# Kernel optimization log

Measured on AMD Instinct MI355X. Metric: run time of the kernel, lower is better.

Reference implementation:

```python
import jax, jax.numpy as jnp
import numpy as np

L, B, T, D, H, DH, DFF, S = 4, 64, 511, 1024, 16, 64, 4096, 256
SCALE = 1.0 / np.sqrt(DH)
EPS = 1e-5


def _ln(x, g, b):
    m = x.mean(-1, keepdims=True)
    v = ((x - m) ** 2).mean(-1, keepdims=True)
    return (x - m) * jax.lax.rsqrt(v + EPS) * g + b


def setup_inputs() -> dict:
    key = jax.random.key(0)
    ks = jax.random.split(key, 24)
    wp = 0.02  # weight init scale to keep activations sane
    r = lambda k, shp, s: jax.random.normal(k, shp, jnp.float32) * s
    return {
        'tgt_last': r(ks[0], (1, B, D), 1.0),
        'cache': r(ks[1], (L, T, B, D), 1.0),
        'K0': r(ks[2], (B, H, T, DH), 1.0),
        'V0': r(ks[3], (B, H, T, DH), 1.0),
        'K_mem': r(ks[4], (L, B, H, S, DH), 1.0),
        'V_mem': r(ks[5], (L, B, H, S, DH), 1.0),
        'sa_W': r(ks[6], (L, 3 * D, D), wp), 'sa_b': r(ks[7], (L, 3 * D), wp),
        'sa_oW': r(ks[8], (L, D, D), wp), 'sa_ob': r(ks[9], (L, D), wp),
        'ca_qW': r(ks[10], (L, D, D), wp), 'ca_qb': r(ks[11], (L, D), wp),
        'ca_oW': r(ks[12], (L, D, D), wp), 'ca_ob': r(ks[13], (L, D), wp),
        'W1': r(ks[14], (L, DFF, D), wp), 'b1': r(ks[15], (L, DFF), wp),
        'W2': r(ks[16], (L, D, DFF), wp), 'b2': r(ks[17], (L, D), wp),
        'ln1_g': jnp.ones((L, D), jnp.float32), 'ln1_b': jnp.zeros((L, D), jnp.float32),
        'ln2_g': jnp.ones((L, D), jnp.float32), 'ln2_b': jnp.zeros((L, D), jnp.float32),
        'ln3_g': jnp.ones((L, D), jnp.float32), 'ln3_b': jnp.zeros((L, D), jnp.float32),
    }


def reference(tgt_last, cache, K0, V0, K_mem, V_mem, sa_W, sa_b, sa_oW, sa_ob,
              ca_qW, ca_qb, ca_oW, ca_ob, W1, b1, W2, b2,
              ln1_g, ln1_b, ln2_g, ln2_b, ln3_g, ln3_b):
    # One incremental decode step through L decoder layers (eval mode, dropout=0).
    x = tgt_last  # [1,B,D]
    for i in range(L):
        last = x
        Wq, Wk, Wv = sa_W[i, :D], sa_W[i, D:2 * D], sa_W[i, 2 * D:]
        bq, bk, bv = sa_b[i, :D], sa_b[i, D:2 * D], sa_b[i, 2 * D:]
        q = (last[0] @ Wq.T + bq).reshape(B, H, DH)  # [B,H,Dh]
        if i == 0:
            # _sa_kv_step: project only the new token, append to cached K/V
            k = (last[0] @ Wk.T + bk).reshape(B, H, 1, DH)
            v = (last[0] @ Wv.T + bv).reshape(B, H, 1, DH)
            K = jnp.concatenate([K0, k], axis=2)  # [B,H,T+1,Dh]
            V = jnp.concatenate([V0, v], axis=2)
        else:
            # standard self-attn: K/V from full prefix concat(cache[i], x)
            tgt_i = jnp.concatenate([cache[i], x], axis=0)  # [T+1,B,D]
            K = (tgt_i @ Wk.T + bk).reshape(T + 1, B, H, DH).transpose(1, 2, 0, 3)
            V = (tgt_i @ Wv.T + bv).reshape(T + 1, B, H, DH).transpose(1, 2, 0, 3)
        s = jnp.einsum('bhd,bhtd->bht', q, K) * SCALE
        a = jax.nn.softmax(s, axis=-1)
        ctx = jnp.einsum('bht,bhtd->bhd', a, V).reshape(B, D)[None]  # [1,B,D]
        sa = ctx @ sa_oW[i].T + sa_ob[i]
        x = _ln(last + sa, ln1_g[i], ln1_b[i])
        # cross-attention against precomputed memory K/V
        qc = (x[0] @ ca_qW[i].T + ca_qb[i]).reshape(B, H, DH)
        sc = jnp.einsum('bhd,bhsd->bhs', qc, K_mem[i]) * SCALE
        ac = jax.nn.softmax(sc, axis=-1)
        cc = jnp.einsum('bhs,bhsd->bhd', ac, V_mem[i]).reshape(B, D)[None]
        cc = cc @ ca_oW[i].T + ca_ob[i]
        x = _ln(x + cc, ln2_g[i], ln2_b[i])
        # FFN (relu, the nn.TransformerDecoderLayer default)
        ff = jax.nn.relu(x @ W1[i].T + b1[i]) @ W2[i].T + b2[i]
        x = _ln(x + ff, ln3_g[i], ln3_b[i])
    return x  # [1,B,D] embedding of the newly decoded token
```

## Files before the change

kernel.cpp:

```cpp
#include <hip/hip_runtime.h>
#include <math.h>

#define B 64
#define D 1024
#define H 16
#define DH 64
#define T 511
#define TT 512
#define SMEM 256
#define DFF 4096
#define NLAYER 4
#define SCALE 0.125f
#define EPS 1e-5f

__device__ __forceinline__ float dot4(const float4 a, const float4 b) {
    return a.x * b.x + a.y * b.y + a.z * b.z + a.w * b.w;
}
__device__ __forceinline__ float4 f4add(float4 a, float4 b) {
    return make_float4(a.x + b.x, a.y + b.y, a.z + b.z, a.w + b.w);
}

template <int K, int KS>
__global__ __launch_bounds__(256) void gemm_proj(
    const float* __restrict__ A,
    const float* __restrict__ W,
    float* __restrict__ P)
{
    constexpr int KSUB = K / KS;
    const int O = gridDim.x * 128;
    const int obase = blockIdx.x * 128;
    const int kb = blockIdx.y * KSUB;
    const int tid = threadIdx.x;

    __shared__ float As[32][68];
    __shared__ float Ws[32][132];

    const int b0 = (tid >> 4) * 4;
    const int o0 = (tid & 15) * 8;

    float acc[4][8];
#pragma unroll
    for (int i = 0; i < 4; ++i)
#pragma unroll
        for (int j = 0; j < 8; ++j) acc[i][j] = 0.f;

    for (int kc = 0; kc < KSUB; kc += 32) {
#pragma unroll
        for (int j = 0; j < 2; ++j) {
            const int f = tid + 256 * j;
            const int bb = f >> 3, k4 = f & 7;
            const float4 v = *reinterpret_cast<const float4*>(
                A + (size_t)bb * K + kb + kc + 4 * k4);
            As[4 * k4 + 0][bb] = v.x; As[4 * k4 + 1][bb] = v.y;
            As[4 * k4 + 2][bb] = v.z; As[4 * k4 + 3][bb] = v.w;
        }
#pragma unroll
        for (int j = 0; j < 4; ++j) {
            const int f = tid + 256 * j;
            const int oo = f >> 3, k4 = f & 7;
            const float4 v = *reinterpret_cast<const float4*>(
                W + (size_t)(obase + oo) * K + kb + kc + 4 * k4);
            Ws[4 * k4 + 0][oo] = v.x; Ws[4 * k4 + 1][oo] = v.y;
            Ws[4 * k4 + 2][oo] = v.z; Ws[4 * k4 + 3][oo] = v.w;
        }
        __syncthreads();
#pragma unroll 8
        for (int k = 0; k < 32; ++k) {
            const float4 av = *reinterpret_cast<const float4*>(&As[k][b0]);
            const float4 w0 = *reinterpret_cast<const float4*>(&Ws[k][o0]);
            const float4 w1 = *reinterpret_cast<const float4*>(&Ws[k][o0 + 4]);
            const float a[4] = {av.x, av.y, av.z, av.w};
            const float w[8] = {w0.x, w0.y, w0.z, w0.w, w1.x, w1.y, w1.z, w1.w};
#pragma unroll
            for (int i = 0; i < 4; ++i)
#pragma unroll
                for (int j = 0; j < 8; ++j)
                    acc[i][j] = fmaf(a[i], w[j], acc[i][j]);
        }
        __syncthreads();
    }

    float* Pb = P + (size_t)blockIdx.y * 64 * O;
#pragma unroll
    for (int i = 0; i < 4; ++i) {
        const float4 v0 = make_float4(acc[i][0], acc[i][1], acc[i][2], acc[i][3]);
        const float4 v1 = make_float4(acc[i][4], acc[i][5], acc[i][6], acc[i][7]);
        *reinterpret_cast<float4*>(Pb + (size_t)(b0 + i) * O + obase + o0) = v0;
        *reinterpret_cast<float4*>(Pb + (size_t)(b0 + i) * O + obase + o0 + 4) = v1;
    }
}

template <int K, int KS, int NPART, bool RELU_A>
__global__ __launch_bounds__(256) void gemm_psum(
    const float* __restrict__ Pa,
    const float* __restrict__ abias,
    const float* __restrict__ W,
    float* __restrict__ P)
{
    constexpr int KSUB = K / KS;
    const int O = gridDim.x * 128;
    const int obase = blockIdx.x * 128;
    const int kb = blockIdx.y * KSUB;
    const int tid = threadIdx.x;

    __shared__ float As[32][68];
    __shared__ float Ws[32][132];

    const int b0 = (tid >> 4) * 4;
    const int o0 = (tid & 15) * 8;

    float acc[4][8];
#pragma unroll
    for (int i = 0; i < 4; ++i)
#pragma unroll
        for (int j = 0; j < 8; ++j) acc[i][j] = 0.f;

    for (int kc = 0; kc < KSUB; kc += 32) {
#pragma unroll
        for (int j = 0; j < 2; ++j) {
            const int f = tid + 256 * j;
            const int bb = f >> 3, k4 = f & 7;
            const int kg = kb + kc + 4 * k4;
            float4 v = *reinterpret_cast<const float4*>(abias + kg);
#pragma unroll
            for (int s = 0; s < NPART; ++s)
                v = f4add(v, *reinterpret_cast<const float4*>(
                    Pa + (size_t)(s * 64 + bb) * K + kg));
            if (RELU_A) {
                v.x = fmaxf(v.x, 0.f); v.y = fmaxf(v.y, 0.f);
                v.z = fmaxf(v.z, 0.f); v.w = fmaxf(v.w, 0.f);
            }
            As[4 * k4 + 0][bb] = v.x; As[4 * k4 + 1][bb] = v.y;
            As[4 * k4 + 2][bb] = v.z; As[4 * k4 + 3][bb] = v.w;
        }
#pragma unroll
        for (int j = 0; j < 4; ++j) {
            const int f = tid + 256 * j;
            const int oo = f >> 3, k4 = f & 7;
            const float4 v = *reinterpret_cast<const float4*>(
                W + (size_t)(obase + oo) * K + kb + kc + 4 * k4);
            Ws[4 * k4 + 0][oo] = v.x; Ws[4 * k4 + 1][oo] = v.y;
            Ws[4 * k4 + 2][oo] = v.z; Ws[4 * k4 + 3][oo] = v.w;
        }
        __syncthreads();
#pragma unroll 8
        for (int k = 0; k < 32; ++k) {
            const float4 av = *reinterpret_cast<const float4*>(&As[k][b0]);
            const float4 w0 = *reinterpret_cast<const float4*>(&Ws[k][o0]);
            const float4 w1 = *reinterpret_cast<const float4*>(&Ws[k][o0 + 4]);
            const float a[4] = {av.x, av.y, av.z, av.w};
            const float w[8] = {w0.x, w0.y, w0.z, w0.w, w1.x, w1.y, w1.z, w1.w};
#pragma unroll
            for (int i = 0; i < 4; ++i)
#pragma unroll
                for (int j = 0; j < 8; ++j)
                    acc[i][j] = fmaf(a[i], w[j], acc[i][j]);
        }
        __syncthreads();
    }

    float* Pb = P + (size_t)blockIdx.y * 64 * O;
#pragma unroll
    for (int i = 0; i < 4; ++i) {
        const float4 v0 = make_float4(acc[i][0], acc[i][1], acc[i][2], acc[i][3]);
        const float4 v1 = make_float4(acc[i][4], acc[i][5], acc[i][6], acc[i][7]);
        *reinterpret_cast<float4*>(Pb + (size_t)(b0 + i) * O + obase + o0) = v0;
        *reinterpret_cast<float4*>(Pb + (size_t)(b0 + i) * O + obase + o0 + 4) = v1;
    }
}

__global__ __launch_bounds__(256) void gemm_u(
    const float* __restrict__ Pq,
    const float* __restrict__ bq,
    const float* __restrict__ Wk,
    float* __restrict__ u)
{
    const int h = blockIdx.x;
    const int dbase = blockIdx.y * 128;
    const int tid = threadIdx.x;

    __shared__ float As[32][68];
    __shared__ float Ws[32][132];

    const int b0 = (tid >> 4) * 4;
    const int o0 = (tid & 15) * 8;

    float acc[4][8];
#pragma unroll
    for (int i = 0; i < 4; ++i)
#pragma unroll
        for (int j = 0; j < 8; ++j) acc[i][j] = 0.f;

    for (int kc = 0; kc < DH; kc += 32) {
#pragma unroll
        for (int j = 0; j < 2; ++j) {
            const int f = tid + 256 * j;
            const int bb = f >> 3, k4 = f & 7;
            const int kg = h * DH + kc + 4 * k4;
            float4 v = *reinterpret_cast<const float4*>(bq + kg);
#pragma unroll
            for (int s = 0; s < 16; ++s)
                v = f4add(v, *reinterpret_cast<const float4*>(
                    Pq + (size_t)(s * 64 + bb) * D + kg));
            As[4 * k4 + 0][bb] = v.x; As[4 * k4 + 1][bb] = v.y;
            As[4 * k4 + 2][bb] = v.z; As[4 * k4 + 3][bb] = v.w;
        }
#pragma unroll
        for (int j = 0; j < 4; ++j) {
            const int f = tid + 256 * j;
            const int k = f >> 5, d4 = f & 31;
            const float4 v = *reinterpret_cast<const float4*>(
                Wk + (size_t)(h * DH + kc + k) * D + dbase + 4 * d4);
            *reinterpret_cast<float4*>(&Ws[k][4 * d4]) = v;
        }
        __syncthreads();
#pragma unroll 8
        for (int k = 0; k < 32; ++k) {
            const float4 av = *reinterpret_cast<const float4*>(&As[k][b0]);
            const float4 w0 = *reinterpret_cast<const float4*>(&Ws[k][o0]);
            const float4 w1 = *reinterpret_cast<const float4*>(&Ws[k][o0 + 4]);
            const float a[4] = {av.x, av.y, av.z, av.w};
            const float w[8] = {w0.x, w0.y, w0.z, w0.w, w1.x, w1.y, w1.z, w1.w};
#pragma unroll
            for (int i = 0; i < 4; ++i)
#pragma unroll
                for (int j = 0; j < 8; ++j)
                    acc[i][j] = fmaf(a[i], w[j], acc[i][j]);
        }
        __syncthreads();
    }
#pragma unroll
    for (int i = 0; i < 4; ++i) {
        const float4 v0 = make_float4(acc[i][0], acc[i][1], acc[i][2], acc[i][3]);
        const float4 v1 = make_float4(acc[i][4], acc[i][5], acc[i][6], acc[i][7]);
        float* ur = u + ((size_t)(b0 + i) * H + h) * D + dbase + o0;
        *reinterpret_cast<float4*>(ur) = v0;
        *reinterpret_cast<float4*>(ur + 4) = v1;
    }
}

__global__ __launch_bounds__(512) void sattn_kernel(
    const float* __restrict__ cache_i, const float* __restrict__ x,
    const float* __restrict__ u, float* __restrict__ wpart4,
    float* __restrict__ sums)
{
    const int b = blockIdx.x, th = blockIdx.y;
    const int tid = threadIdx.x;
    const int h = tid >> 5, seg = tid & 31;

    float4 ur[8];
    const float* ub = u + ((size_t)(b * H + h)) * D;
#pragma unroll
    for (int c = 0; c < 8; ++c) {
        const float4 v = *reinterpret_cast<const float4*>(ub + c * 128 + seg * 4);
        ur[c] = make_float4(v.x * SCALE, v.y * SCALE, v.z * SCALE, v.w * SCALE);
    }
    float4 ar[8];
#pragma unroll
    for (int c = 0; c < 8; ++c) ar[c] = make_float4(0.f, 0.f, 0.f, 0.f);
    float sumE = 0.f;

    __shared__ float rowb[2][2][1024];

    const int tg0 = th * 128;
    const int lr = tid >> 8;
    const int lc = (tid & 255) * 4;

    auto rowptr = [&](int t) -> const float* {
        return (t < T) ? cache_i + ((size_t)t * B + b) * D : x + (size_t)b * D;
    };
    float4 pre = *reinterpret_cast<const float4*>(rowptr(tg0 + lr) + lc);

    for (int st = 0; st < 64; ++st) {
        const int p = st & 1;
        *reinterpret_cast<float4*>(&rowb[p][lr][lc]) = pre;
        __syncthreads();
        if (st + 1 < 64)
            pre = *reinterpret_cast<const float4*>(
                rowptr(tg0 + 2 * (st + 1) + lr) + lc);
#pragma unroll
        for (int r = 0; r < 2; ++r) {
            float4 rv[8];
            float dot = 0.f;
#pragma unroll
            for (int c = 0; c < 8; ++c) {
                rv[c] = *reinterpret_cast<const float4*>(
                    &rowb[p][r][c * 128 + seg * 4]);
                dot += dot4(ur[c], rv[c]);
            }
#pragma unroll
            for (int m = 16; m >= 1; m >>= 1) dot += __shfl_xor(dot, m, 64);
            const float e = __expf(dot);
            sumE += e;
#pragma unroll
            for (int c = 0; c < 8; ++c) {
                ar[c].x = fmaf(e, rv[c].x, ar[c].x);
                ar[c].y = fmaf(e, rv[c].y, ar[c].y);
                ar[c].z = fmaf(e, rv[c].z, ar[c].z);
                ar[c].w = fmaf(e, rv[c].w, ar[c].w);
            }
        }
    }

    float* wp = wpart4 + (((size_t)(b * 4 + th)) * H + h) * D;
#pragma unroll
    for (int c = 0; c < 8; ++c)
        *reinterpret_cast<float4*>(wp + c * 128 + seg * 4) = ar[c];
    if (seg == 0) sums[(b * 4 + th) * H + h] = sumE;
}

__global__ __launch_bounds__(256) void gemm_ctx8(
    const float* __restrict__ wpart4, const float* __restrict__ sums,
    const float* __restrict__ Wv, float* __restrict__ P)
{
    constexpr int KSUB = D / 8;
    const int h = blockIdx.x;
    const int kb = blockIdx.y * KSUB;
    const int tid = threadIdx.x;

    __shared__ float As[32][68];
    __shared__ float Ws[32][68];
    __shared__ float sinv[64];

    if (tid < 64) {
        float s = 0.f;
#pragma unroll
        for (int t = 0; t < 4; ++t) s += sums[(tid * 4 + t) * H + h];
        sinv[tid] = 1.f / s;
    }
    __syncthreads();

    const int b0 = (tid >> 4) * 4;
    const int o0 = (tid & 15) * 4;

    float acc[4][4];
#pragma unroll
    for (int i = 0; i < 4; ++i)
#pragma unroll
        for (int j = 0; j < 4; ++j) acc[i][j] = 0.f;

    for (int kc = 0; kc < KSUB; kc += 32) {
#pragma unroll
        for (int j = 0; j < 2; ++j) {
            const int f = tid + 256 * j;
            const int bb = f >> 3, k4 = f & 7;
            const int kg = kb + kc + 4 * k4;
            float4 v = make_float4(0.f, 0.f, 0.f, 0.f);
#pragma unroll
            for (int t = 0; t < 4; ++t)
                v = f4add(v, *reinterpret_cast<const float4*>(
                    wpart4 + (((size_t)(bb * 4 + t)) * H + h) * D + kg));
            const float iv = sinv[bb];
            As[4 * k4 + 0][bb] = v.x * iv; As[4 * k4 + 1][bb] = v.y * iv;
            As[4 * k4 + 2][bb] = v.z * iv; As[4 * k4 + 3][bb] = v.w * iv;
        }
#pragma unroll
        for (int j = 0; j < 2; ++j) {
            const int f = tid + 256 * j;
            const int oo = f >> 3, k4 = f & 7;
            const float4 v = *reinterpret_cast<const float4*>(
                Wv + (size_t)(h * DH + oo) * D + kb + kc + 4 * k4);
            Ws[4 * k4 + 0][oo] = v.x; Ws[4 * k4 + 1][oo] = v.y;
            Ws[4 * k4 + 2][oo] = v.z; Ws[4 * k4 + 3][oo] = v.w;
        }
        __syncthreads();
#pragma unroll 8
        for (int k = 0; k < 32; ++k) {
            const float4 av = *reinterpret_cast<const float4*>(&As[k][b0]);
            const float4 wv = *reinterpret_cast<const float4*>(&Ws[k][o0]);
            const float a[4] = {av.x, av.y, av.z, av.w};
            const float w[4] = {wv.x, wv.y, wv.z, wv.w};
#pragma unroll
            for (int i = 0; i < 4; ++i)
#pragma unroll
                for (int j = 0; j < 4; ++j)
                    acc[i][j] = fmaf(a[i], w[j], acc[i][j]);
        }
        __syncthreads();
    }
    float* Pb = P + (size_t)blockIdx.y * 64 * D;
#pragma unroll
    for (int i = 0; i < 4; ++i) {
        const float4 v = make_float4(acc[i][0], acc[i][1], acc[i][2], acc[i][3]);
        *reinterpret_cast<float4*>(Pb + (size_t)(b0 + i) * D + h * DH + o0) = v;
    }
}

template <int KS>
__global__ __launch_bounds__(256) void finish_ln(
    const float* __restrict__ P, const float* __restrict__ bias,
    const float* __restrict__ resid, const float* __restrict__ g,
    const float* __restrict__ bb, float* __restrict__ out)
{
    const int b = blockIdx.x, tid = threadIdx.x;
    const float4* P4 = reinterpret_cast<const float4*>(P);
    float4 v = reinterpret_cast<const float4*>(bias)[tid];
    v = f4add(v, reinterpret_cast<const float4*>(resid + (size_t)b * D)[tid]);
#pragma unroll
    for (int s = 0; s < KS; ++s)
        v = f4add(v, P4[(size_t)(s * 64 + b) * 256 + tid]);

    float ssum = v.x + v.y + v.z + v.w;
#pragma unroll
    for (int m = 32; m >= 1; m >>= 1) ssum += __shfl_xor(ssum, m, 64);
    __shared__ float red[4];
    if ((tid & 63) == 0) red[tid >> 6] = ssum;
    __syncthreads();
    const float mean = (red[0] + red[1] + red[2] + red[3]) * (1.f / D);
    const float dx = v.x - mean, dy = v.y - mean, dz = v.z - mean, dw = v.w - mean;
    float q = dx * dx + dy * dy + dz * dz + dw * dw;
#pragma unroll
    for (int m = 32; m >= 1; m >>= 1) q += __shfl_xor(q, m, 64);
    __shared__ float red2[4];
    if ((tid & 63) == 0) red2[tid >> 6] = q;
    __syncthreads();
    const float var = (red2[0] + red2[1] + red2[2] + red2[3]) * (1.f / D);
    const float rs = rsqrtf(var + EPS);
    const float4 gv = reinterpret_cast<const float4*>(g)[tid];
    const float4 bv = reinterpret_cast<const float4*>(bb)[tid];
    float4 o;
    o.x = dx * rs * gv.x + bv.x;
    o.y = dy * rs * gv.y + bv.y;
    o.z = dz * rs * gv.z + bv.z;
    o.w = dw * rs * gv.w + bv.w;
    reinterpret_cast<float4*>(out + (size_t)b * D)[tid] = o;
}

template <int NS, bool HASX>
__global__ __launch_bounds__(256) void attn_kernel(
    const float* __restrict__ qP, const float* __restrict__ qbias,
    int qnp, int qpitch,
    const float* __restrict__ Kb, const float* __restrict__ Vb,
    float* __restrict__ ctx, int nk)
{
    const int b = blockIdx.x, h = blockIdx.y, tid = threadIdx.x;
    __shared__ float qs[DH];
    __shared__ float kx[DH];
    __shared__ float vx[DH];
    __shared__ float sa[NS];
    if (tid < DH) {
        const int col = h * DH + tid;
        float v = qbias[col];
        for (int s = 0; s < qnp; ++s)
            v += qP[(size_t)(s * 64 + b) * qpitch + col];
        qs[tid] = v;
        if (HASX) {
            float kk = qbias[D + col];
            float vv = qbias[2 * D + col];
            for (int s = 0; s < qnp; ++s) {
                const float* base = qP + (size_t)(s * 64 + b) * qpitch + col;
                kk += base[D];
                vv += base[2 * D];
            }
            kx[tid] = kk; vx[tid] = vv;
        }
    }
    __syncthreads();

    const int ss = tid >> 2, p = tid & 3;
    const float* Kbh = Kb + ((size_t)(b * H + h)) * nk * DH;
#pragma unroll 2
    for (int pass = 0; pass < NS / 64; ++pass) {
        const int s = pass * 64 + ss;
        const float* row = (!HASX || s < nk) ? (Kbh + (size_t)s * DH)
                                             : (const float*)kx;
        const float4* rp = reinterpret_cast<const float4*>(row);
        const float4* qp = reinterpret_cast<const float4*>(qs) + p * 4;
        float acc = 0.f;
#pragma unroll
        for (int c = 0; c < 4; ++c) acc += dot4(rp[p * 4 + c], qp[c]);
        acc += __shfl_xor(acc, 1, 64);
        acc += __shfl_xor(acc, 2, 64);
        if (p == 0) sa[s] = acc * SCALE;
    }
    __syncthreads();

    float m = -1e30f;
    for (int k = tid; k < NS; k += 256) m = fmaxf(m, sa[k]);
#pragma unroll
    for (int mm = 32; mm >= 1; mm >>= 1) m = fmaxf(m, __shfl_xor(m, mm, 64));
    __shared__ float r1[4];
    if ((tid & 63) == 0) r1[tid >> 6] = m;
    __syncthreads();
    m = fmaxf(fmaxf(r1[0], r1[1]), fmaxf(r1[2], r1[3]));
    float sum = 0.f;
    for (int k = tid; k < NS; k += 256) {
        const float e = __expf(sa[k] - m);
        sa[k] = e;
        sum += e;
    }
#pragma unroll
    for (int mm = 32; mm >= 1; mm >>= 1) sum += __shfl_xor(sum, mm, 64);
    __shared__ float r2[4];
    if ((tid & 63) == 0) r2[tid >> 6] = sum;
    __syncthreads();
    const float inv = 1.f / (r2[0] + r2[1] + r2[2] + r2[3]);

    const int dh4 = tid & 15, sq = tid >> 4;
    const float* Vbh = Vb + ((size_t)(b * H + h)) * nk * DH;
    float4 acc = make_float4(0.f, 0.f, 0.f, 0.f);
#pragma unroll 2
    for (int s = sq; s < NS; s += 16) {
        const float* row = (!HASX || s < nk) ? (Vbh + (size_t)s * DH)
                                             : (const float*)vx;
        const float4 vv = *reinterpret_cast<const float4*>(row + dh4 * 4);
        const float av = sa[s];
        acc.x += av * vv.x; acc.y += av * vv.y;
        acc.z += av * vv.z; acc.w += av * vv.w;
    }
    __shared__ float red[16 * 68];
    *reinterpret_cast<float4*>(&red[sq * 68 + dh4 * 4]) = acc;
    __syncthreads();
    if (tid < 64) {
        float t = 0.f;
#pragma unroll
        for (int k = 0; k < 16; ++k) t += red[k * 68 + tid];
        ctx[(size_t)b * D + h * DH + tid] = t * inv;
    }
}

extern "C" void kernel_launch(void* const* d_in, const int* in_sizes, int n_in,
                              void* d_out, int out_size, void* d_ws, size_t ws_size,
                              hipStream_t stream)
{
    const float* tgt_last = (const float*)d_in[0];
    const float* cache    = (const float*)d_in[1];
    const float* K0       = (const float*)d_in[2];
    const float* V0       = (const float*)d_in[3];
    const float* K_mem    = (const float*)d_in[4];
    const float* V_mem    = (const float*)d_in[5];
    const float* sa_W     = (const float*)d_in[6];
    const float* sa_b     = (const float*)d_in[7];
    const float* sa_oW    = (const float*)d_in[8];
    const float* sa_ob    = (const float*)d_in[9];
    const float* ca_qW    = (const float*)d_in[10];
    const float* ca_qb    = (const float*)d_in[11];
    const float* ca_oW    = (const float*)d_in[12];
    const float* ca_ob    = (const float*)d_in[13];
    const float* W1       = (const float*)d_in[14];
    const float* b1       = (const float*)d_in[15];
    const float* W2       = (const float*)d_in[16];
    const float* b2       = (const float*)d_in[17];
    const float* ln1_g    = (const float*)d_in[18];
    const float* ln1_b    = (const float*)d_in[19];
    const float* ln2_g    = (const float*)d_in[20];
    const float* ln2_b    = (const float*)d_in[21];
    const float* ln3_g    = (const float*)d_in[22];
    const float* ln3_b    = (const float*)d_in[23];

    float* ws = (float*)d_ws;
    float* x_buf   = ws;
    float* ctx_buf = ws + 65536;
    float* u_buf   = ws + 131072;
    float* wpart4  = ws + 1179648;
    float* sums    = ws + 5373952;
    float* Pq      = ws + 5378048;
    float* PqA     = ws + 6426624;
    float* Pqkv    = ws + 8523776;
    float* Pc      = ws + 10096640;
    float* Pffn    = ws + 10620928;
    float* Pffn2   = ws + 12718080;

    const dim3 blk(256);

    for (int i = 0; i < NLAYER; ++i) {
        const float* Wq   = sa_W + (size_t)i * 3 * D * D;
        const float* bqkv = sa_b + (size_t)i * 3 * D;

        if (i == 0) {
            gemm_proj<D, 8><<<dim3(24, 8), blk, 0, stream>>>(tgt_last, Wq, Pqkv);
            attn_kernel<TT, true><<<dim3(B, H), blk, 0, stream>>>(
                Pqkv, bqkv, 8, 3 * D, K0, V0, ctx_buf, T);
            gemm_proj<D, 32><<<dim3(8, 32), blk, 0, stream>>>(
                ctx_buf, sa_oW + (size_t)i * D * D, PqA);
            finish_ln<32><<<dim3(B), blk, 0, stream>>>(
                PqA, sa_ob + (size_t)i * D, tgt_last,
                ln1_g + (size_t)i * D, ln1_b + (size_t)i * D, x_buf);
        } else {
            const float* cache_i = cache + (size_t)i * T * B * D;
            gemm_proj<D, 16><<<dim3(8, 16), blk, 0, stream>>>(x_buf, Wq, Pq);
            gemm_u<<<dim3(H, 8), blk, 0, stream>>>(
                Pq, bqkv, Wq + (size_t)D * D, u_buf);
            sattn_kernel<<<dim3(B, 4), dim3(512), 0, stream>>>(
                cache_i, x_buf, u_buf, wpart4, sums);
            gemm_ctx8<<<dim3(H, 8), blk, 0, stream>>>(
                wpart4, sums, Wq + (size_t)2 * D * D, Pc);
            gemm_psum<D, 32, 8, false><<<dim3(8, 32), blk, 0, stream>>>(
                Pc, bqkv + 2 * D, sa_oW + (size_t)i * D * D, PqA);
            finish_ln<32><<<dim3(B), blk, 0, stream>>>(
                PqA, sa_ob + (size_t)i * D, x_buf,
                ln1_g + (size_t)i * D, ln1_b + (size_t)i * D, x_buf);
        }

        gemm_proj<D, 32><<<dim3(8, 32), blk, 0, stream>>>(
            x_buf, ca_qW + (size_t)i * D * D, PqA);
        attn_kernel<SMEM, false><<<dim3(B, H), blk, 0, stream>>>(
            PqA, ca_qb + (size_t)i * D, 32, D,
            K_mem + (size_t)i * B * H * SMEM * DH,
            V_mem + (size_t)i * B * H * SMEM * DH, ctx_buf, SMEM);
        gemm_proj<D, 32><<<dim3(8, 32), blk, 0, stream>>>(
            ctx_buf, ca_oW + (size_t)i * D * D, PqA);
        finish_ln<32><<<dim3(B), blk, 0, stream>>>(
            PqA, ca_ob + (size_t)i * D, x_buf,
            ln2_g + (size_t)i * D, ln2_b + (size_t)i * D, x_buf);

        gemm_proj<D, 8><<<dim3(32, 8), blk, 0, stream>>>(
            x_buf, W1 + (size_t)i * DFF * D, Pffn);
        gemm_psum<DFF, 32, 8, true><<<dim3(8, 32), blk, 0, stream>>>(
            Pffn, b1 + (size_t)i * DFF, W2 + (size_t)i * D * DFF, Pffn2);
        float* lnout = (i == NLAYER - 1) ? (float*)d_out : x_buf;
        finish_ln<32><<<dim3(B), blk, 0, stream>>>(
            Pffn2, b2 + (size_t)i * D, x_buf,
            ln3_g + (size_t)i * D, ln3_b + (size_t)i * D, lnout);
    }
}
```

Measured before the change: 937.6 us.

## Increase split-K parallelism and process two heads per thread in self-attention

The self-attention scan kernel now splits the time axis into 8 chunks instead of 4 and uses 256-thread blocks. Each thread handles two heads, so every cached row loaded into shared memory is reused twice from registers. The FFN and first-layer QKV GEMMs get more K-splits (16/64 partials) for more blocks, and attn_kernel reduces the query/K/V partial sums across all 256 threads instead of 64. The costs are larger partial buffers, more reduction traffic in the consumer kernels and higher register pressure.

```diff
diff --git a/kernel.cpp b/kernel.cpp
--- a/kernel.cpp
+++ b/kernel.cpp
@@ -22,8 +22,7 @@
 
 template <int K, int KS>
 __global__ __launch_bounds__(256) void gemm_proj(
-    const float* __restrict__ A,
-    const float* __restrict__ W,
+    const float* __restrict__ A, const float* __restrict__ W,
     float* __restrict__ P)
 {
     constexpr int KSUB = K / KS;
@@ -92,10 +91,8 @@
 
 template <int K, int KS, int NPART, bool RELU_A>
 __global__ __launch_bounds__(256) void gemm_psum(
-    const float* __restrict__ Pa,
-    const float* __restrict__ abias,
-    const float* __restrict__ W,
-    float* __restrict__ P)
+    const float* __restrict__ Pa, const float* __restrict__ abias,
+    const float* __restrict__ W, float* __restrict__ P)
 {
     constexpr int KSUB = K / KS;
     const int O = gridDim.x * 128;
@@ -170,10 +167,8 @@
 }
 
 __global__ __launch_bounds__(256) void gemm_u(
-    const float* __restrict__ Pq,
-    const float* __restrict__ bq,
-    const float* __restrict__ Wk,
-    float* __restrict__ u)
+    const float* __restrict__ Pq, const float* __restrict__ bq,
+    const float* __restrict__ Wk, float* __restrict__ u)
 {
     const int h = blockIdx.x;
     const int dbase = blockIdx.y * 128;
@@ -209,9 +204,9 @@
         for (int j = 0; j < 4; ++j) {
             const int f = tid + 256 * j;
             const int k = f >> 5, d4 = f & 31;
-            const float4 v = *reinterpret_cast<const float4*>(
-                Wk + (size_t)(h * DH + kc + k) * D + dbase + 4 * d4);
-            *reinterpret_cast<float4*>(&Ws[k][4 * d4]) = v;
+            *reinterpret_cast<float4*>(&Ws[k][4 * d4]) =
+                *reinterpret_cast<const float4*>(
+                    Wk + (size_t)(h * DH + kc + k) * D + dbase + 4 * d4);
         }
         __syncthreads();
 #pragma unroll 8
@@ -239,83 +234,104 @@
     }
 }
 
-__global__ __launch_bounds__(512) void sattn_kernel(
+__global__ __launch_bounds__(256) void sattn_kernel(
     const float* __restrict__ cache_i, const float* __restrict__ x,
-    const float* __restrict__ u, float* __restrict__ wpart4,
-    float* __restrict__ sums)
-{
-    const int b = blockIdx.x, th = blockIdx.y;
+    const float* __restrict__ u, float* __restrict__ wp8,
+    float* __restrict__ sums8)
+{
+    const int b = blockIdx.x, t8 = blockIdx.y;
     const int tid = threadIdx.x;
-    const int h = tid >> 5, seg = tid & 31;
-
-    float4 ur[8];
-    const float* ub = u + ((size_t)(b * H + h)) * D;
+    const int hp = tid >> 5;
+    const int h0 = hp * 2, h1 = h0 + 1;
+    const int seg = tid & 31;
+    const int dof = seg * 4;
+
+    float4 u0[8], u1[8], a0[8], a1[8];
+    const float* ub0 = u + ((size_t)(b * H + h0)) * D;
+    const float* ub1 = u + ((size_t)(b * H + h1)) * D;
 #pragma unroll
     for (int c = 0; c < 8; ++c) {
-        const float4 v = *reinterpret_cast<const float4*>(ub + c * 128 + seg * 4);
-        ur[c] = make_float4(v.x * SCALE, v.y * SCALE, v.z * SCALE, v.w * SCALE);
-    }
-    float4 ar[8];
-#pragma unroll
-    for (int c = 0; c < 8; ++c) ar[c] = make_float4(0.f, 0.f, 0.f, 0.f);
-    float sumE = 0.f;
+        float4 v = *reinterpret_cast<const float4*>(ub0 + c * 128 + dof);
+        u0[c] = make_float4(v.x * SCALE, v.y * SCALE, v.z * SCALE, v.w * SCALE);
+        v = *reinterpret_cast<const float4*>(ub1 + c * 128 + dof);
+        u1[c] = make_float4(v.x * SCALE, v.y * SCALE, v.z * SCALE, v.w * SCALE);
+        a0[c] = make_float4(0.f, 0.f, 0.f, 0.f);
+        a1[c] = make_float4(0.f, 0.f, 0.f, 0.f);
+    }
+    float s0 = 0.f, s1 = 0.f;
 
     __shared__ float rowb[2][2][1024];
-
-    const int tg0 = th * 128;
-    const int lr = tid >> 8;
-    const int lc = (tid & 255) * 4;
+    const int tg0 = t8 * 64;
+    const int lr = tid >> 7;
+    const int lcf = (tid & 127) * 8;
 
     auto rowptr = [&](int t) -> const float* {
         return (t < T) ? cache_i + ((size_t)t * B + b) * D : x + (size_t)b * D;
     };
-    float4 pre = *reinterpret_cast<const float4*>(rowptr(tg0 + lr) + lc);
-
-    for (int st = 0; st < 64; ++st) {
+    float4 pa = *reinterpret_cast<const float4*>(rowptr(tg0 + lr) + lcf);
+    float4 pb = *reinterpret_cast<const float4*>(rowptr(tg0 + lr) + lcf + 4);
+
+    for (int st = 0; st < 32; ++st) {
         const int p = st & 1;
-        *reinterpret_cast<float4*>(&rowb[p][lr][lc]) = pre;
-        __syncthreads();
-        if (st + 1 < 64)
-            pre = *reinterpret_cast<const float4*>(
-                rowptr(tg0 + 2 * (st + 1) + lr) + lc);
+        *reinterpret_cast<float4*>(&rowb[p][lr][lcf]) = pa;
+        *reinterpret_cast<float4*>(&rowb[p][lr][lcf + 4]) = pb;
+        __syncthreads();
+        if (st + 1 < 32) {
+            const int t = tg0 + 2 * (st + 1) + lr;
+            pa = *reinterpret_cast<const float4*>(rowptr(t) + lcf);
+            pb = *reinterpret_cast<const float4*>(rowptr(t) + lcf + 4);
+        }
 #pragma unroll
         for (int r = 0; r < 2; ++r) {
+            const float* rowp = &rowb[p][r][0];
             float4 rv[8];
-            float dot = 0.f;
+            float d0 = 0.f, d1 = 0.f;
 #pragma unroll
             for (int c = 0; c < 8; ++c) {
-                rv[c] = *reinterpret_cast<const float4*>(
-                    &rowb[p][r][c * 128 + seg * 4]);
-                dot += dot4(ur[c], rv[c]);
+                rv[c] = *reinterpret_cast<const float4*>(rowp + c * 128 + dof);
+                d0 += dot4(u0[c], rv[c]);
+                d1 += dot4(u1[c], rv[c]);
             }
 #pragma unroll
-            for (int m = 16; m >= 1; m >>= 1) dot += __shfl_xor(dot, m, 64);
-            const float e = __expf(dot);
-            sumE += e;
+            for (int m = 16; m >= 1; m >>= 1) {
+                d0 += __shfl_xor(d0, m, 64);
+                d1 += __shfl_xor(d1, m, 64);
+            }
+            const float e0 = __expf(d0), e1 = __expf(d1);
+            s0 += e0; s1 += e1;
 #pragma unroll
             for (int c = 0; c < 8; ++c) {
-                ar[c].x = fmaf(e, rv[c].x, ar[c].x);
-                ar[c].y = fmaf(e, rv[c].y, ar[c].y);
-                ar[c].z = fmaf(e, rv[c].z, ar[c].z);
-                ar[c].w = fmaf(e, rv[c].w, ar[c].w);
+                a0[c].x = fmaf(e0, rv[c].x, a0[c].x);
+                a0[c].y = fmaf(e0, rv[c].y, a0[c].y);
+                a0[c].z = fmaf(e0, rv[c].z, a0[c].z);
+                a0[c].w = fmaf(e0, rv[c].w, a0[c].w);
+                a1[c].x = fmaf(e1, rv[c].x, a1[c].x);
+                a1[c].y = fmaf(e1, rv[c].y, a1[c].y);
+                a1[c].z = fmaf(e1, rv[c].z, a1[c].z);
+                a1[c].w = fmaf(e1, rv[c].w, a1[c].w);
             }
         }
     }
 
-    float* wp = wpart4 + (((size_t)(b * 4 + th)) * H + h) * D;
-#pragma unroll
-    for (int c = 0; c < 8; ++c)
-        *reinterpret_cast<float4*>(wp + c * 128 + seg * 4) = ar[c];
-    if (seg == 0) sums[(b * 4 + th) * H + h] = sumE;
+    float* w0 = wp8 + ((size_t)((b * 8 + t8) * H + h0)) * D;
+    float* w1 = wp8 + ((size_t)((b * 8 + t8) * H + h1)) * D;
+#pragma unroll
+    for (int c = 0; c < 8; ++c) {
+        *reinterpret_cast<float4*>(w0 + c * 128 + dof) = a0[c];
+        *reinterpret_cast<float4*>(w1 + c * 128 + dof) = a1[c];
+    }
+    if (seg == 0) {
+        sums8[(b * 8 + t8) * H + h0] = s0;
+        sums8[(b * 8 + t8) * H + h1] = s1;
+    }
 }
 
 __global__ __launch_bounds__(256) void gemm_ctx8(
-    const float* __restrict__ wpart4, const float* __restrict__ sums,
+    const float* __restrict__ wp8, const float* __restrict__ sums8,
     const float* __restrict__ Wv, float* __restrict__ P)
 {
-    constexpr int KSUB = D / 8;
     const int h = blockIdx.x;
-    const int kb = blockIdx.y * KSUB;
+    const int kb = blockIdx.y * 128;
     const int tid = threadIdx.x;
 
     __shared__ float As[32][68];
@@ -325,7 +341,7 @@
     if (tid < 64) {
         float s = 0.f;
 #pragma unroll
-        for (int t = 0; t < 4; ++t) s += sums[(tid * 4 + t) * H + h];
+        for (int t = 0; t < 8; ++t) s += sums8[(tid * 8 + t) * H + h];
         sinv[tid] = 1.f / s;
     }
     __syncthreads();
@@ -339,7 +355,7 @@
 #pragma unroll
         for (int j = 0; j < 4; ++j) acc[i][j] = 0.f;
 
-    for (int kc = 0; kc < KSUB; kc += 32) {
+    for (int kc = 0; kc < 128; kc += 32) {
 #pragma unroll
         for (int j = 0; j < 2; ++j) {
             const int f = tid + 256 * j;
@@ -347,9 +363,9 @@
             const int kg = kb + kc + 4 * k4;
             float4 v = make_float4(0.f, 0.f, 0.f, 0.f);
 #pragma unroll
-            for (int t = 0; t < 4; ++t)
+            for (int t = 0; t < 8; ++t)
                 v = f4add(v, *reinterpret_cast<const float4*>(
-                    wpart4 + (((size_t)(bb * 4 + t)) * H + h) * D + kg));
+                    wp8 + ((size_t)((bb * 8 + t) * H + h)) * D + kg));
             const float iv = sinv[bb];
             As[4 * k4 + 0][bb] = v.x * iv; As[4 * k4 + 1][bb] = v.y * iv;
             As[4 * k4 + 2][bb] = v.z * iv; As[4 * k4 + 3][bb] = v.w * iv;
@@ -426,38 +442,49 @@
     reinterpret_cast<float4*>(out + (size_t)b * D)[tid] = o;
 }
 
-template <int NS, bool HASX>
+template <int NS, bool HASX, int NPART, int QP>
 __global__ __launch_bounds__(256) void attn_kernel(
     const float* __restrict__ qP, const float* __restrict__ qbias,
-    int qnp, int qpitch,
     const float* __restrict__ Kb, const float* __restrict__ Vb,
     float* __restrict__ ctx, int nk)
 {
     const int b = blockIdx.x, h = blockIdx.y, tid = threadIdx.x;
-    __shared__ float qs[DH];
-    __shared__ float kx[DH];
-    __shared__ float vx[DH];
+    __shared__ float qs[DH], kx[DH], vx[DH];
     __shared__ float sa[NS];
-    if (tid < DH) {
-        const int col = h * DH + tid;
-        float v = qbias[col];
-        for (int s = 0; s < qnp; ++s)
-            v += qP[(size_t)(s * 64 + b) * qpitch + col];
-        qs[tid] = v;
+    __shared__ float red[1088];
+    __shared__ float r1[4], r2[4];
+
+    {
+        const int grp = tid >> 6, col = tid & 63;
+        constexpr int NP4 = NPART / 4;
+        const int colg = h * DH + col;
+        float aq = 0.f, ak = 0.f, av = 0.f;
+#pragma unroll
+        for (int s = 0; s < NP4; ++s) {
+            const float* base = qP + (size_t)((grp * NP4 + s) * 64 + b) * QP + colg;
+            aq += base[0];
+            if (HASX) { ak += base[D]; av += base[2 * D]; }
+        }
+        red[grp * 64 + col] = aq;
         if (HASX) {
-            float kk = qbias[D + col];
-            float vv = qbias[2 * D + col];
-            for (int s = 0; s < qnp; ++s) {
-                const float* base = qP + (size_t)(s * 64 + b) * qpitch + col;
-                kk += base[D];
-                vv += base[2 * D];
+            red[256 + grp * 64 + col] = ak;
+            red[512 + grp * 64 + col] = av;
+        }
+        __syncthreads();
+        if (tid < 64) {
+            qs[tid] = qbias[h * DH + tid] + red[tid] + red[64 + tid] +
+                      red[128 + tid] + red[192 + tid];
+            if (HASX) {
+                kx[tid] = qbias[D + h * DH + tid] + red[256 + tid] +
+                          red[320 + tid] + red[384 + tid] + red[448 + tid];
+                vx[tid] = qbias[2 * D + h * DH + tid] + red[512 + tid] +
+                          red[576 + tid] + red[640 + tid] + red[704 + tid];
             }
-            kx[tid] = kk; vx[tid] = vv;
-        }
-    }
-    __syncthreads();
-
-    const int ss = tid >> 2, p = tid & 3;
+        }
+        __syncthreads();
+    }
+
+    const int ss = tid >> 2, pp = tid & 3;
     const float* Kbh = Kb + ((size_t)(b * H + h)) * nk * DH;
 #pragma unroll 2
     for (int pass = 0; pass < NS / 64; ++pass) {
@@ -465,13 +492,13 @@
         const float* row = (!HASX || s < nk) ? (Kbh + (size_t)s * DH)
                                              : (const float*)kx;
         const float4* rp = reinterpret_cast<const float4*>(row);
-        const float4* qp = reinterpret_cast<const float4*>(qs) + p * 4;
+        const float4* qp = reinterpret_cast<const float4*>(qs);
         float acc = 0.f;
 #pragma unroll
-        for (int c = 0; c < 4; ++c) acc += dot4(rp[p * 4 + c], qp[c]);
+        for (int c = 0; c < 4; ++c) acc += dot4(rp[pp * 4 + c], qp[pp * 4 + c]);
         acc += __shfl_xor(acc, 1, 64);
         acc += __shfl_xor(acc, 2, 64);
-        if (p == 0) sa[s] = acc * SCALE;
+        if (pp == 0) sa[s] = acc * SCALE;
     }
     __syncthreads();
 
@@ -479,7 +506,6 @@
     for (int k = tid; k < NS; k += 256) m = fmaxf(m, sa[k]);
 #pragma unroll
     for (int mm = 32; mm >= 1; mm >>= 1) m = fmaxf(m, __shfl_xor(m, mm, 64));
-    __shared__ float r1[4];
     if ((tid & 63) == 0) r1[tid >> 6] = m;
     __syncthreads();
     m = fmaxf(fmaxf(r1[0], r1[1]), fmaxf(r1[2], r1[3]));
@@ -491,7 +517,6 @@
     }
 #pragma unroll
     for (int mm = 32; mm >= 1; mm >>= 1) sum += __shfl_xor(sum, mm, 64);
-    __shared__ float r2[4];
     if ((tid & 63) == 0) r2[tid >> 6] = sum;
     __syncthreads();
     const float inv = 1.f / (r2[0] + r2[1] + r2[2] + r2[3]);
@@ -504,11 +529,11 @@
         const float* row = (!HASX || s < nk) ? (Vbh + (size_t)s * DH)
                                              : (const float*)vx;
         const float4 vv = *reinterpret_cast<const float4*>(row + dh4 * 4);
-        const float av = sa[s];
-        acc.x += av * vv.x; acc.y += av * vv.y;
-        acc.z += av * vv.z; acc.w += av * vv.w;
-    }
-    __shared__ float red[16 * 68];
+        const float aw = sa[s];
+        acc.x += aw * vv.x; acc.y += aw * vv.y;
+        acc.z += aw * vv.z; acc.w += aw * vv.w;
+    }
+    __syncthreads();
     *reinterpret_cast<float4*>(&red[sq * 68 + dh4 * 4]) = acc;
     __syncthreads();
     if (tid < 64) {
@@ -549,68 +574,70 @@
     const float* ln3_b    = (const float*)d_in[23];
 
     float* ws = (float*)d_ws;
-    float* x_buf   = ws;
-    float* ctx_buf = ws + 65536;
-    float* u_buf   = ws + 131072;
-    float* wpart4  = ws + 1179648;
-    float* sums    = ws + 5373952;
-    float* Pq      = ws + 5378048;
-    float* PqA     = ws + 6426624;
-    float* Pqkv    = ws + 8523776;
-    float* Pc      = ws + 10096640;
-    float* Pffn    = ws + 10620928;
-    float* Pffn2   = ws + 12718080;
+    float* x_buf  = ws;
+    float* ctx_b  = ws + 65536;
+    float* u_buf  = ws + 131072;
+    float* wp8    = ws + 1179648;
+    float* sums8  = ws + 9568256;
+    float* Pq     = ws + 9576448;
+    float* Pqkv   = ws + 10625024;
+    float* Pc     = ws + 13770752;
+    float* PA     = ws + 14295040;
+    float* Pf1    = ws + 16392192;
+    float* Pf2    = ws + 20586496;
 
     const dim3 blk(256);
 
     for (int i = 0; i < NLAYER; ++i) {
-        const float* Wq   = sa_W + (size_t)i * 3 * D * D;
+        const float* Wqkv = sa_W + (size_t)i * 3 * D * D;
         const float* bqkv = sa_b + (size_t)i * 3 * D;
+        const float* xin = (i == 0) ? tgt_last : x_buf;
 
         if (i == 0) {
-            gemm_proj<D, 8><<<dim3(24, 8), blk, 0, stream>>>(tgt_last, Wq, Pqkv);
-            attn_kernel<TT, true><<<dim3(B, H), blk, 0, stream>>>(
-                Pqkv, bqkv, 8, 3 * D, K0, V0, ctx_buf, T);
-            gemm_proj<D, 32><<<dim3(8, 32), blk, 0, stream>>>(
-                ctx_buf, sa_oW + (size_t)i * D * D, PqA);
-            finish_ln<32><<<dim3(B), blk, 0, stream>>>(
-                PqA, sa_ob + (size_t)i * D, tgt_last,
-                ln1_g + (size_t)i * D, ln1_b + (size_t)i * D, x_buf);
+            gemm_proj<D, 16><<<dim3(24, 16), blk, 0, stream>>>(tgt_last, Wqkv, Pqkv);
+            attn_kernel<TT, true, 16, 3 * D><<<dim3(B, H), blk, 0, stream>>>(
+                Pqkv, bqkv, K0, V0, ctx_b, T);
         } else {
             const float* cache_i = cache + (size_t)i * T * B * D;
-            gemm_proj<D, 16><<<dim3(8, 16), blk, 0, stream>>>(x_buf, Wq, Pq);
+            gemm_proj<D, 16><<<dim3(8, 16), blk, 0, stream>>>(x_buf, Wqkv, Pq);
             gemm_u<<<dim3(H, 8), blk, 0, stream>>>(
-                Pq, bqkv, Wq + (size_t)D * D, u_buf);
-            sattn_kernel<<<dim3(B, 4), dim3(512), 0, stream>>>(
-                cache_i, x_buf, u_buf, wpart4, sums);
+                Pq, bqkv, Wqkv + (size_t)D * D, u_buf);
+            sattn_kernel<<<dim3(B, 8), blk, 0, stream>>>(
+                cache_i, x_buf, u_buf, wp8, sums8);
             gemm_ctx8<<<dim3(H, 8), blk, 0, stream>>>(
-                wpart4, sums, Wq + (size_t)2 * D * D, Pc);
+                wp8, sums8, Wqkv + (size_t)2 * D * D, Pc);
+        }
+
+        if (i == 0) {
+            gemm_proj<D, 32><<<dim3(8, 32), blk, 0, stream>>>(
+                ctx_b, sa_oW + (size_t)i * D * D, PA);
+        } else {
             gemm_psum<D, 32, 8, false><<<dim3(8, 32), blk, 0, stream>>>(
-                Pc, bqkv + 2 * D, sa_oW + (size_t)i * D * D, PqA);
-            finish_ln<32><<<dim3(B), blk, 0, stream>>>(
-                PqA, sa_ob + (size_t)i * D, x_buf,
-                ln1_g + (size_t)i * D, ln1_b + (size_t)i * D, x_buf);
-        }
+                Pc, bqkv + 2 * D, sa_oW + (size_t)i * D * D, PA);
+        }
+        finish_ln<32><<<dim3(B), blk, 0, stream>>>(
+            PA, sa_ob + (size_t)i * D, xin,
+            ln1_g + (size_t)i * D, ln1_b + (size_t)i * D, x_buf);
 
         gemm_proj<D, 32><<<dim3(8, 32), blk, 0, stream>>>(
-            x_buf, ca_qW + (size_t)i * D * D, PqA);
-        attn_kernel<SMEM, false><<<dim3(B, H), blk, 0, stream>>>(
-            PqA, ca_qb + (size_t)i * D, 32, D,
+            x_buf, ca_qW + (size_t)i * D * D, PA);
+        attn_kernel<SMEM, false, 32, D><<<dim3(B, H), blk, 0, stream>>>(
+            PA, ca_qb + (size_t)i * D,
             K_mem + (size_t)i * B * H * SMEM * DH,
-            V_mem + (size_t)i * B * H * SMEM * DH, ctx_buf, SMEM);
+            V_mem + (size_t)i * B * H * SMEM * DH, ctx_b, SMEM);
         gemm_proj<D, 32><<<dim3(8, 32), blk, 0, stream>>>(
-            ctx_buf, ca_oW + (size_t)i * D * D, PqA);
+            ctx_b, ca_oW + (size_t)i * D * D, PA);
         finish_ln<32><<<dim3(B), blk, 0, stream>>>(
-            PqA, ca_ob + (size_t)i * D, x_buf,
+            PA, ca_ob + (size_t)i * D, x_buf,
             ln2_g + (size_t)i * D, ln2_b + (size_t)i * D, x_buf);
 
-        gemm_proj<D, 8><<<dim3(32, 8), blk, 0, stream>>>(
-            x_buf, W1 + (size_t)i * DFF * D, Pffn);
-        gemm_psum<DFF, 32, 8, true><<<dim3(8, 32), blk, 0, stream>>>(
-            Pffn, b1 + (size_t)i * DFF, W2 + (size_t)i * D * DFF, Pffn2);
+        gemm_proj<D, 16><<<dim3(32, 16), blk, 0, stream>>>(
+            x_buf, W1 + (size_t)i * DFF * D, Pf1);
+        gemm_psum<DFF, 64, 16, true><<<dim3(8, 64), blk, 0, stream>>>(
+            Pf1, b1 + (size_t)i * DFF, W2 + (size_t)i * D * DFF, Pf2);
         float* lnout = (i == NLAYER - 1) ? (float*)d_out : x_buf;
-        finish_ln<32><<<dim3(B), blk, 0, stream>>>(
-            Pffn2, b2 + (size_t)i * D, x_buf,
+        finish_ln<64><<<dim3(B), blk, 0, stream>>>(
+            Pf2, b2 + (size_t)i * D, x_buf,
             ln3_g + (size_t)i * D, ln3_b + (size_t)i * D, lnout);
     }
 }
```

Result: faster. 807.0 us (median of 2 runs) (-13.9%).
